# Optimization experiments

Measured on AMD Instinct MI355X. Metric: run time of the kernel, lower is better.

The kernel has to match this reference:

```python
import jax, jax.numpy as jnp
import numpy as np

# Dims: B=4 batch, S=1024 seq, E=512 embed_dim, H=8 heads, K=3 gate lookback.
_B, _S, _E, _H, _K = 4, 1024, 512, 8, 3
_EPS_LN = 1e-5
_DIV_DELTA = 1e-12


def setup_inputs() -> dict:
    key = jax.random.key(0)
    ks = jax.random.split(key, 8)

    def w(k, shape, s=0.02):
        return jax.random.normal(k, shape, jnp.float32) * s

    return {
        "query": jax.random.normal(ks[0], (_B, _S, _E), jnp.float32),
        "ln1_g": jnp.ones((_E,), jnp.float32),
        "ln1_b": jnp.zeros((_E,), jnp.float32),
        "in_proj_w": w(ks[1], (3 * _E, _E)),          # packed W_q;W_k;W_v
        "in_proj_b": jnp.zeros((3 * _E,), jnp.float32),
        "out_w": w(ks[2], (_E, _H * _E)),             # out_proj: Linear(E*H -> E)
        "out_b": jnp.zeros((_E,), jnp.float32),
        "conv_w": w(ks[3], (_H, _E, _K)),             # SyntacticDistanceGate causal conv
        "conv_b": jnp.zeros((_H,), jnp.float32),
        "ln2_g": jnp.ones((_E,), jnp.float32),
        "ln2_b": jnp.zeros((_E,), jnp.float32),
        "mlp_w1": w(ks[4], (4 * _E, _E)),
        "mlp_b1": jnp.zeros((4 * _E,), jnp.float32),
        "mlp_w2": w(ks[5], (_E, 4 * _E)),
        "mlp_b2": jnp.zeros((_E,), jnp.float32),
    }


def _layer_norm(x, g, b):
    m = jnp.mean(x, axis=-1, keepdims=True)
    v = jnp.mean(jnp.square(x - m), axis=-1, keepdims=True)
    return (x - m) * jax.lax.rsqrt(v + _EPS_LN) * g + b


def _syntactic_gate(x, conv_w, conv_b):
    """x: [B,S,E] -> gate [B,H,S,S], distance [B,H,S].
    Causal depth-to-head conv produces per-head syntactic distances; gate is a
    smooth comparison sigmoid(d_i - d_j) (PRPN-style distance gating)."""
    K = conv_w.shape[-1]
    xp = jnp.pad(x, ((0, 0), (K - 1, 0), (0, 0)))  # causal left pad
    S = x.shape[1]
    d = conv_b[None, :, None]
    for k in range(K):  # tiny fixed lookback loop
        d = d + jnp.einsum("bse,he->bhs", xp[:, k:k + S, :], conv_w[:, :, k])
    distance = jnp.tanh(d)                               # [B,H,S]
    gate = jax.nn.sigmoid(distance[:, :, :, None] - distance[:, :, None, :])
    return gate, distance


def reference(query, ln1_g, ln1_b, in_proj_w, in_proj_b, out_w, out_b,
              conv_w, conv_b, ln2_g, ln2_b, mlp_w1, mlp_b1, mlp_w2, mlp_b2):
    B, S, E = query.shape
    H = conv_w.shape[0]

    nq = _layer_norm(query, ln1_g, ln1_b)  # self-attention: key=value=normed query

    gate, _distance = _syntactic_gate(nq, conv_w, conv_b)  # [B,H,S,S]

    # In-projections (heads are NOT split: each head sees full E-dim q/k/v).
    qkv = nq @ in_proj_w.T + in_proj_b          # [B,S,3E]
    q, k, v = jnp.split(qkv, 3, axis=-1)

    # Raw scores (scaled by sqrt(E), per source). Identical across heads since
    # q/k are merely repeated per head; compute once and broadcast over H.
    scores = jnp.einsum("bie,bje->bij", q, k) / jnp.sqrt(jnp.float32(E))

    # NOTE: with no key_padding_mask the source skips softmax entirely; the
    # gate multiplies RAW scores, then sum-normalizes.
    w = scores[:, None, :, :] * gate                       # [B,H,S,S]
    w = w / (jnp.sum(w, axis=-1, keepdims=True) + _DIV_DELTA)

    ctx = jnp.einsum("bhij,bje->bhie", w, v)               # [B,H,S,E]
    # torch: chunk over head-major dim 0 then cat on features -> [B,S,H*E]
    ctx = jnp.transpose(ctx, (0, 2, 1, 3)).reshape(B, S, H * E)
    attn_out = ctx @ out_w.T + out_b                       # [B,S,E]

    x = query + attn_out                                   # layer_scale_1 = Identity
    h = _layer_norm(x, ln2_g, ln2_b)
    h = jax.nn.gelu(h @ mlp_w1.T + mlp_b1, approximate=False)
    x = x + (h @ mlp_w2.T + mlp_b2)                        # layer_scale_2 = Identity
    return x
```

## Files before the change

### kernel.cpp

```cpp
#include <hip/hip_runtime.h>
#include <math.h>

#define SQ 1024
#define EE 512
#define NB 4
#define NH 8

typedef __attribute__((ext_vector_type(8))) short bfrag;
typedef __attribute__((ext_vector_type(4))) float f32x4;
typedef __attribute__((ext_vector_type(4))) unsigned short u16x4;
typedef __attribute__((ext_vector_type(8))) unsigned short u16x8;

typedef __attribute__((address_space(3))) unsigned int lds_u32;
typedef const __attribute__((address_space(1))) unsigned int glb_u32;

__device__ __forceinline__ float sep(float x) {
  asm volatile("" : "+v"(x));
  return x;
}

__device__ __forceinline__ unsigned short f2bf(float f) {
  unsigned u = __builtin_bit_cast(unsigned, f);
  unsigned r = (u + 0x7fffu + ((u >> 16) & 1u)) >> 16;
  return (unsigned short)r;
}
__device__ __forceinline__ float bf2f(unsigned short h) {
  unsigned u = ((unsigned)h) << 16;
  return __builtin_bit_cast(float, u);
}

__device__ __forceinline__ void split4(float4 v, u16x4& h, u16x4& l) {
  h.x = f2bf(v.x); l.x = f2bf(v.x - bf2f(h.x));
  h.y = f2bf(v.y); l.y = f2bf(v.y - bf2f(h.y));
  h.z = f2bf(v.z); l.z = f2bf(v.z - bf2f(h.z));
  h.w = f2bf(v.w); l.w = f2bf(v.w - bf2f(h.w));
}

__device__ __forceinline__ int swzi(int row, int c8) {
  return row * 40 + ((c8 ^ ((row >> 2) & 6)) << 2);
}

__global__ __launch_bounds__(64) void ln_np(const float* __restrict__ x,
                                            const float* __restrict__ g,
                                            const float* __restrict__ b,
                                            float* __restrict__ y) {
  __shared__ float xs[EE];
  __shared__ float bc[2];
  long long t = blockIdx.x;
  int lane = threadIdx.x;
#pragma unroll
  for (int m = 0; m < 8; m++) xs[lane + 64 * m] = x[t * EE + lane + 64 * m];
  __syncthreads();
  int l = lane >> 3, a = lane & 7;
  float r = 0.f;
  if (lane < 32) {
    r = xs[l * 128 + a];
#pragma unroll
    for (int m = 1; m < 16; m++) r = r + xs[l * 128 + 8 * m + a];
  }
  r = r + __shfl_xor(r, 1);
  r = r + __shfl_xor(r, 2);
  r = r + __shfl_xor(r, 4);
  r = r + __shfl_xor(r, 8);
  r = r + __shfl_xor(r, 16);
  if (lane == 0) bc[0] = r / 512.0f;
  __syncthreads();
  float mean = bc[0];
  r = 0.f;
  if (lane < 32) {
#pragma unroll
    for (int m = 0; m < 16; m++) {
      float d = sep(xs[l * 128 + 8 * m + a] - mean);
      float s2 = sep(d * d);
      r = (m == 0) ? s2 : (r + s2);
    }
  }
  r = r + __shfl_xor(r, 1);
  r = r + __shfl_xor(r, 2);
  r = r + __shfl_xor(r, 4);
  r = r + __shfl_xor(r, 8);
  r = r + __shfl_xor(r, 16);
  if (lane == 0) bc[1] = r / 512.0f;
  __syncthreads();
  float var = bc[1];
  float rs = 1.0f / sqrtf(var + 1e-5f);
#pragma unroll
  for (int m = 0; m < 8; m++) {
    int i = lane + 64 * m;
    float d = sep(xs[i] - mean);
    float t1 = sep(d * rs);
    float t2 = sep(t1 * g[i]);
    y[t * EE + i] = t2 + b[i];
  }
}

__global__ __launch_bounds__(64) void ln_np_s(const float* __restrict__ x,
                                              const float* __restrict__ g,
                                              const float* __restrict__ b,
                                              unsigned short* __restrict__ yh,
                                              unsigned short* __restrict__ yl) {
  __shared__ float xs[EE];
  __shared__ float bc[2];
  long long t = blockIdx.x;
  int lane = threadIdx.x;
#pragma unroll
  for (int m = 0; m < 8; m++) xs[lane + 64 * m] = x[t * EE + lane + 64 * m];
  __syncthreads();
  int l = lane >> 3, a = lane & 7;
  float r = 0.f;
  if (lane < 32) {
    r = xs[l * 128 + a];
#pragma unroll
    for (int m = 1; m < 16; m++) r = r + xs[l * 128 + 8 * m + a];
  }
  r = r + __shfl_xor(r, 1);
  r = r + __shfl_xor(r, 2);
  r = r + __shfl_xor(r, 4);
  r = r + __shfl_xor(r, 8);
  r = r + __shfl_xor(r, 16);
  if (lane == 0) bc[0] = r / 512.0f;
  __syncthreads();
  float mean = bc[0];
  r = 0.f;
  if (lane < 32) {
#pragma unroll
    for (int m = 0; m < 16; m++) {
      float d = sep(xs[l * 128 + 8 * m + a] - mean);
      float s2 = sep(d * d);
      r = (m == 0) ? s2 : (r + s2);
    }
  }
  r = r + __shfl_xor(r, 1);
  r = r + __shfl_xor(r, 2);
  r = r + __shfl_xor(r, 4);
  r = r + __shfl_xor(r, 8);
  r = r + __shfl_xor(r, 16);
  if (lane == 0) bc[1] = r / 512.0f;
  __syncthreads();
  float var = bc[1];
  float rs = 1.0f / sqrtf(var + 1e-5f);
#pragma unroll
  for (int m = 0; m < 8; m++) {
    int i = lane + 64 * m;
    float d = sep(xs[i] - mean);
    float t1 = sep(d * rs);
    float t2 = sep(t1 * g[i]);
    float o = t2 + b[i];
    unsigned short hh = f2bf(o);
    yh[t * EE + i] = hh;
    yl[t * EE + i] = f2bf(o - bf2f(hh));
  }
}

__global__ __launch_bounds__(256) void dist_np(const float* __restrict__ nq,
                                               const float* __restrict__ conv_w,
                                               const float* __restrict__ conv_b,
                                               float* __restrict__ dist) {
  int bh = blockIdx.x;
  int b = bh >> 3, h = bh & 7;
  float cb = conv_b[h];
  const float* W = conv_w + (long long)h * EE * 3;
  int s = blockIdx.y * 256 + threadIdx.x;
  float d = cb;
#pragma unroll
  for (int k = 0; k < 3; k++) {
    int t = s - 2 + k;
    if (t < 0) continue;
    const float* row = nq + ((long long)b * SQ + t) * EE;
    float acc = 0.f;
    for (int e = 0; e < EE; e++) acc = __builtin_fmaf(row[e], W[e * 3 + k], acc);
    d = sep(d + acc);
  }
  dist[(long long)bh * SQ + s] = (float)tanh((double)d);
}

__device__ __forceinline__ float gelu_exact(float x) {
  return 0.5f * x * (1.f + erff(x / 1.41421356237309504880f));
}

template <int ACT, int SPLITK>
__global__ __launch_bounds__(256) void gemm_nt(const float* __restrict__ A, int lda, long long sA,
                                               const float* __restrict__ B, int ldb, long long sB,
                                               const float* __restrict__ bias,
                                               const float* __restrict__ Res,
                                               float* __restrict__ C, int ldc, long long sC,
                                               int K, float alpha) {
  __shared__ float As[16][68];
  __shared__ float Bs[16][68];
  int z = blockIdx.z;
  A += (long long)z * sA;
  B += (long long)z * sB;
  C += (long long)z * sC;
  int m0 = blockIdx.y * 64, n0 = blockIdx.x * 64;
  int tid = threadIdx.x;
  int lr = tid >> 2, lc = tid & 3;
  int tx = tid & 15, ty = tid >> 4;
  float acc[4][4] = {};
  float acc2[4][4] = {};
  const float* Arow = A + (long long)(m0 + lr) * lda + lc * 4;
  const float* Brow = B + (long long)(n0 + lr) * ldb + lc * 4;
  float4 a4 = *(const float4*)(Arow);
  float4 b4 = *(const float4*)(Brow);
  for (int k0 = 0; k0 < K; k0 += 16) {
    __syncthreads();
    As[lc * 4 + 0][lr] = a4.x; As[lc * 4 + 1][lr] = a4.y;
    As[lc * 4 + 2][lr] = a4.z; As[lc * 4 + 3][lr] = a4.w;
    Bs[lc * 4 + 0][lr] = b4.x; Bs[lc * 4 + 1][lr] = b4.y;
    Bs[lc * 4 + 2][lr] = b4.z; Bs[lc * 4 + 3][lr] = b4.w;
    __syncthreads();
    int kn = (k0 + 16 < K) ? (k0 + 16) : k0;
    float4 a4n = *(const float4*)(Arow + kn);
    float4 b4n = *(const float4*)(Brow + kn);
    float(*tgt)[4] = (SPLITK > 0 && k0 >= SPLITK) ? acc2 : acc;
#pragma unroll
    for (int kk = 0; kk < 16; kk++) {
      float4 av = *(const float4*)&As[kk][ty * 4];
      float4 bv = *(const float4*)&Bs[kk][tx * 4];
      float a[4] = {av.x, av.y, av.z, av.w};
      float bb[4] = {bv.x, bv.y, bv.z, bv.w};
#pragma unroll
      for (int i = 0; i < 4; i++)
#pragma unroll
        for (int j = 0; j < 4; j++) tgt[i][j] += a[i] * bb[j];
    }
    a4 = a4n;
    b4 = b4n;
  }
  if (SPLITK > 0) {
#pragma unroll
    for (int i = 0; i < 4; i++)
#pragma unroll
      for (int j = 0; j < 4; j++) acc[i][j] = sep(acc[i][j]) + acc2[i][j];
  }
  float4 bias4 = make_float4(0.f, 0.f, 0.f, 0.f);
  if (ACT != 2 && bias) bias4 = *(const float4*)(bias + n0 + tx * 4);
#pragma unroll
  for (int i = 0; i < 4; i++) {
    int row = m0 + ty * 4 + i;
    float o[4];
    if (ACT == 2) {
#pragma unroll
      for (int j = 0; j < 4; j++) o[j] = acc[i][j] / alpha;
    } else {
      o[0] = sep(acc[i][0] * alpha) + bias4.x;
      o[1] = sep(acc[i][1] * alpha) + bias4.y;
      o[2] = sep(acc[i][2] * alpha) + bias4.z;
      o[3] = sep(acc[i][3] * alpha) + bias4.w;
    }
    if (ACT == 1) {
#pragma unroll
      for (int j = 0; j < 4; j++) o[j] = gelu_exact(o[j]);
    }
    if (Res) {
      float4 r4 = *(const float4*)(Res + (long long)row * ldc + n0 + tx * 4);
      o[0] = sep(o[0]) + r4.x; o[1] = sep(o[1]) + r4.y;
      o[2] = sep(o[2]) + r4.z; o[3] = sep(o[3]) + r4.w;
    }
    *(float4*)(C + (long long)row * ldc + n0 + tx * 4) = make_float4(o[0], o[1], o[2], o[3]);
  }
}

__global__ __launch_bounds__(64) void rowsum_np(const float* __restrict__ scores,
                                                const float* __restrict__ dist,
                                                float* __restrict__ invrs) {
  __shared__ float wsm[SQ];
  int i = blockIdx.x;
  int z = blockIdx.y;
  int b = z >> 3;
  const float* srow = scores + ((long long)b * SQ + i) * SQ;
  const float* dz = dist + (long long)z * SQ;
  float di = dz[i];
  int lane = threadIdx.x;
#pragma unroll
  for (int m = 0; m < 16; m++) {
    int j = lane + 64 * m;
    float e = (float)exp((double)(dz[j] - di));
    float gg = 1.f / (1.f + e);
    wsm[j] = srow[j] * gg;
  }
  __syncthreads();
  int l = lane >> 3, a = lane & 7;
  float r = wsm[l * 128 + a];
#pragma unroll
  for (int m = 1; m < 16; m++) r = r + wsm[l * 128 + 8 * m + a];
  r = r + __shfl_xor(r, 1);
  r = r + __shfl_xor(r, 2);
  r = r + __shfl_xor(r, 4);
  r = r + __shfl_xor(r, 8);
  r = r + __shfl_xor(r, 16);
  r = r + __shfl_xor(r, 32);
  if (lane == 0) invrs[(long long)z * SQ + i] = 1.f / (r + 1e-12f);
}

__global__ __launch_bounds__(256) void vsplit_t(const float* __restrict__ qkv,
                                                unsigned short* __restrict__ VhT,
                                                unsigned short* __restrict__ VlT) {
  __shared__ float tile[64][65];
  int b = blockIdx.z;
  int j0 = blockIdx.x * 64;
  int e0 = blockIdx.y * 64;
  const float* V = qkv + (long long)b * SQ * (3 * EE) + 2 * EE;
  unsigned short* Vh = VhT + (long long)b * EE * SQ;
  unsigned short* Vl = VlT + (long long)b * EE * SQ;
  int tx = threadIdx.x & 15, ty = threadIdx.x >> 4;
#pragma unroll
  for (int r = 0; r < 4; r++) {
    int j = j0 + ty + r * 16;
    float4 v = *(const float4*)(V + (long long)j * (3 * EE) + e0 + tx * 4);
    tile[ty + r * 16][tx * 4 + 0] = v.x;
    tile[ty + r * 16][tx * 4 + 1] = v.y;
    tile[ty + r * 16][tx * 4 + 2] = v.z;
    tile[ty + r * 16][tx * 4 + 3] = v.w;
  }
  __syncthreads();
#pragma unroll
  for (int r = 0; r < 4; r++) {
    int el = ty + r * 16;
    float4 f;
    f.x = tile[tx * 4 + 0][el];
    f.y = tile[tx * 4 + 1][el];
    f.z = tile[tx * 4 + 2][el];
    f.w = tile[tx * 4 + 3][el];
    u16x4 hh, ll;
    split4(f, hh, ll);
    long long o = (long long)(e0 + el) * SQ + j0 + tx * 4;
    *(u16x4*)(Vh + o) = hh;
    *(u16x4*)(Vl + o) = ll;
  }
}

__global__ __launch_bounds__(256) void wsplit(const float* __restrict__ W,
                                              unsigned short* __restrict__ Wh,
                                              unsigned short* __restrict__ Wl, int n4) {
  int i = blockIdx.x * 256 + threadIdx.x;
  if (i >= n4) return;
  float4 v = *(const float4*)(W + (long long)i * 4);
  u16x4 h, l;
  split4(v, h, l);
  *(u16x4*)(Wh + (long long)i * 4) = h;
  *(u16x4*)(Wl + (long long)i * 4) = l;
}

__global__ __launch_bounds__(256) void ctx_bf3(const float* __restrict__ scores,
                                               const float* __restrict__ dist,
                                               const float* __restrict__ invrs,
                                               const unsigned short* __restrict__ VhT,
                                               const unsigned short* __restrict__ VlT,
                                               unsigned short* __restrict__ Ch,
                                               unsigned short* __restrict__ Cl) {
  constexpr int BN = 256;
  constexpr int NF = 4;
  __shared__ __align__(16) unsigned short Ah[64 * 40], Al[64 * 40];
  __shared__ __align__(16) unsigned short Bh[BN * 40], Bl[BN * 40];
  int z = blockIdx.z, b = z >> 3, h = z & 7;
  const float* Sb = scores + (long long)b * SQ * SQ;
  const unsigned short* Vh = VhT + (long long)b * EE * SQ;
  const unsigned short* Vl = VlT + (long long)b * EE * SQ;
  unsigned short* Chb = Ch + (long long)b * SQ * (NH * EE) + h * EE;
  unsigned short* Clb = Cl + (long long)b * SQ * (NH * EE) + h * EE;
  const float* dz = dist + (long long)z * SQ;
  int m0 = blockIdx.y * 64, n0 = blockIdx.x * BN;
  int tid = threadIdx.x;
  int wave = tid >> 6, lane = tid & 63;
  int quad = lane >> 4, l16 = lane & 15;
  int colb0 = wave * 64;
  f32x4 acc[4][NF];
#pragma unroll
  for (int mf = 0; mf < 4; mf++)
#pragma unroll
    for (int nf = 0; nf < NF; nf++) acc[mf][nf] = (f32x4)(0.f);

  int aam = tid & 63, aakc = tid >> 6;
  float di = dz[m0 + aam];
  float inv = invrs[(long long)z * SQ + m0 + aam];
  const float* Srow = Sb + (long long)(m0 + aam) * SQ;
  int brow = tid;
  const unsigned short* VhRow = Vh + (long long)(n0 + brow) * SQ;
  const unsigned short* VlRow = Vl + (long long)(n0 + brow) * SQ;

  u16x4 aH[2], aL[2];
  u16x8 bH[4], bL[4];

  auto loadconv = [&](int kb) {
#pragma unroll
    for (int r = 0; r < 2; r++) {
      int kc = aakc + r * 4;
      float4 s4 = *(const float4*)(Srow + kb + kc * 4);
      float4 d4 = *(const float4*)(dz + kb + kc * 4);
      float4 a;
      a.x = (s4.x * __builtin_amdgcn_rcpf(1.f + __expf(d4.x - di))) * inv;
      a.y = (s4.y * __builtin_amdgcn_rcpf(1.f + __expf(d4.y - di))) * inv;
      a.z = (s4.z * __builtin_amdgcn_rcpf(1.f + __expf(d4.z - di))) * inv;
      a.w = (s4.w * __builtin_amdgcn_rcpf(1.f + __expf(d4.w - di))) * inv;
      split4(a, aH[r], aL[r]);
    }
#pragma unroll
    for (int c = 0; c < 4; c++) {
      bH[c] = *(const u16x8*)(VhRow + kb + c * 8);
      bL[c] = *(const u16x8*)(VlRow + kb + c * 8);
    }
  };

  loadconv(0);
  for (int k0 = 0; k0 < SQ; k0 += 32) {
    __syncthreads();
#pragma unroll
    for (int r = 0; r < 2; r++) {
      *(u16x4*)&Ah[swzi(aam, aakc + r * 4)] = aH[r];
      *(u16x4*)&Al[swzi(aam, aakc + r * 4)] = aL[r];
    }
#pragma unroll
    for (int c = 0; c < 4; c++) {
      *(u16x8*)&Bh[swzi(brow, 2 * c)] = bH[c];
      *(u16x8*)&Bl[swzi(brow, 2 * c)] = bL[c];
    }
    __syncthreads();
    int kn = (k0 + 32 < SQ) ? (k0 + 32) : k0;
    loadconv(kn);
    bfrag bhf[NF], blf[NF];
#pragma unroll
    for (int nf = 0; nf < NF; nf++) {
      bhf[nf] = *(const bfrag*)&Bh[swzi(colb0 + nf * 16 + l16, quad * 2)];
      blf[nf] = *(const bfrag*)&Bl[swzi(colb0 + nf * 16 + l16, quad * 2)];
    }
#pragma unroll
    for (int mf = 0; mf < 4; mf++) {
      bfrag ah = *(const bfrag*)&Ah[swzi(mf * 16 + l16, quad * 2)];
      bfrag al = *(const bfrag*)&Al[swzi(mf * 16 + l16, quad * 2)];
#pragma unroll
      for (int nf = 0; nf < NF; nf++) {
        acc[mf][nf] = __builtin_amdgcn_mfma_f32_16x16x32_bf16(al, bhf[nf], acc[mf][nf], 0, 0, 0);
        acc[mf][nf] = __builtin_amdgcn_mfma_f32_16x16x32_bf16(ah, blf[nf], acc[mf][nf], 0, 0, 0);
        acc[mf][nf] = __builtin_amdgcn_mfma_f32_16x16x32_bf16(ah, bhf[nf], acc[mf][nf], 0, 0, 0);
      }
    }
  }
#pragma unroll
  for (int mf = 0; mf < 4; mf++) {
#pragma unroll
    for (int nf = 0; nf < NF; nf++) {
      int col = n0 + colb0 + nf * 16 + l16;
#pragma unroll
      for (int r = 0; r < 4; r++) {
        int row = m0 + mf * 16 + quad * 4 + r;
        float o = acc[mf][nf][r];
        unsigned short hh = f2bf(o);
        Chb[(long long)row * (NH * EE) + col] = hh;
        Clb[(long long)row * (NH * EE) + col] = f2bf(o - bf2f(hh));
      }
    }
  }
}

template <int ACT, int OUTM>
__global__ __launch_bounds__(256) void gemm_bf3s(
    const unsigned short* __restrict__ Ah_g, const unsigned short* __restrict__ Al_g, int lda,
    const unsigned short* __restrict__ Bh_g, const unsigned short* __restrict__ Bl_g, int ldb,
    const float* __restrict__ bias, const float* __restrict__ Res,
    float* __restrict__ C, unsigned short* __restrict__ Ch, unsigned short* __restrict__ Cl,
    int ldc, int K) {
  __shared__ __align__(16) unsigned short lds[3][4][64 * 32];
  int gx = gridDim.x;
  int nwg = gx * (int)gridDim.y;
  int lin = blockIdx.y * gx + blockIdx.x;
  int cpx = nwg >> 3;
  int tl = (lin & 7) * cpx + (lin >> 3);
  int bx = tl % gx, by = tl / gx;
  int m0 = by * 64, n0 = bx * 64;
  int tid = threadIdx.x, wave = tid >> 6, lane = tid & 63;
  int quad = lane >> 4, l16 = lane & 15;
  int colb0 = wave * 16;

  const unsigned short* gsrc = (wave == 0) ? Ah_g : (wave == 1) ? Al_g : (wave == 2) ? Bh_g : Bl_g;
  int gld = (wave < 2) ? lda : ldb;
  int grow0 = (wave < 2) ? m0 : n0;
  long long gbase[4];
#pragma unroll
  for (int qt = 0; qt < 4; qt++) {
    int row = qt * 16 + (lane >> 2);
    int cG = (lane & 3) ^ ((row >> 1) & 3);
    gbase[qt] = (long long)(grow0 + row) * gld + cG * 8;
  }

  auto stage = [&](int buf, int kb) {
#pragma unroll
    for (int qt = 0; qt < 4; qt++) {
      const unsigned short* gp = gsrc + gbase[qt] + kb;
      unsigned short* lp = &lds[buf][wave][qt * 512];
      __builtin_amdgcn_global_load_lds((glb_u32*)gp, (lds_u32*)lp, 16, 0, 0);
    }
  };

  int aoff[4], boff;
#pragma unroll
  for (int mf = 0; mf < 4; mf++) {
    int r = mf * 16 + l16;
    aoff[mf] = r * 32 + ((quad ^ ((r >> 1) & 3)) * 8);
  }
  {
    int r = colb0 + l16;
    boff = r * 32 + ((quad ^ ((r >> 1) & 3)) * 8);
  }

  f32x4 acc[4];
#pragma unroll
  for (int mf = 0; mf < 4; mf++) acc[mf] = (f32x4)(0.f);

  int NT = K >> 5;
  stage(0, 0);
  stage(1, 32);
  int cur = 0;
  for (int t = 0; t < NT; t++) {
    int nb = cur + 2; if (nb >= 3) nb -= 3;
    int kf = (t + 2 < NT) ? (t + 2) * 32 : (NT - 1) * 32;
    stage(nb, kf);
    asm volatile("s_waitcnt vmcnt(8)" ::: "memory");
    __builtin_amdgcn_s_barrier();
    __builtin_amdgcn_sched_barrier(0);
    const unsigned short* Lah = lds[cur][0];
    const unsigned short* Lal = lds[cur][1];
    const unsigned short* Lbh = lds[cur][2];
    const unsigned short* Lbl = lds[cur][3];
    bfrag bh = *(const bfrag*)&Lbh[boff];
    bfrag bl = *(const bfrag*)&Lbl[boff];
#pragma unroll
    for (int mf = 0; mf < 4; mf++) {
      bfrag ah = *(const bfrag*)&Lah[aoff[mf]];
      bfrag al = *(const bfrag*)&Lal[aoff[mf]];
      acc[mf] = __builtin_amdgcn_mfma_f32_16x16x32_bf16(al, bh, acc[mf], 0, 0, 0);
      acc[mf] = __builtin_amdgcn_mfma_f32_16x16x32_bf16(ah, bl, acc[mf], 0, 0, 0);
      acc[mf] = __builtin_amdgcn_mfma_f32_16x16x32_bf16(ah, bh, acc[mf], 0, 0, 0);
    }
    __builtin_amdgcn_sched_barrier(0);
    __builtin_amdgcn_s_barrier();
    cur++; if (cur >= 3) cur -= 3;
  }

  int col = n0 + colb0 + l16;
  float bi = bias ? bias[col] : 0.f;
#pragma unroll
  for (int mf = 0; mf < 4; mf++) {
#pragma unroll
    for (int r = 0; r < 4; r++) {
      int row = m0 + mf * 16 + quad * 4 + r;
      float o = acc[mf][r] + bi;
      if (ACT == 1) o = gelu_exact(o);
      if (OUTM == 0) {
        if (Res) o = o + Res[(long long)row * ldc + col];
        C[(long long)row * ldc + col] = o;
      } else {
        unsigned short hh = f2bf(o);
        Ch[(long long)row * ldc + col] = hh;
        Cl[(long long)row * ldc + col] = f2bf(o - bf2f(hh));
      }
    }
  }
}

extern "C" void kernel_launch(void* const* d_in, const int* in_sizes, int n_in,
                              void* d_out, int out_size, void* d_ws, size_t ws_size,
                              hipStream_t stream) {
  const float* query     = (const float*)d_in[0];
  const float* ln1_g     = (const float*)d_in[1];
  const float* ln1_b     = (const float*)d_in[2];
  const float* in_proj_w = (const float*)d_in[3];
  const float* in_proj_b = (const float*)d_in[4];
  const float* out_w     = (const float*)d_in[5];
  const float* out_b     = (const float*)d_in[6];
  const float* conv_w    = (const float*)d_in[7];
  const float* conv_b    = (const float*)d_in[8];
  const float* ln2_g     = (const float*)d_in[9];
  const float* ln2_b     = (const float*)d_in[10];
  const float* mlp_w1    = (const float*)d_in[11];
  const float* mlp_b1    = (const float*)d_in[12];
  const float* mlp_w2    = (const float*)d_in[13];
  const float* mlp_b2    = (const float*)d_in[14];
  float* out = (float*)d_out;
  char* ws = (char*)d_ws;

  float* nq     = (float*)(ws + 0);
  float* qkv    = (float*)(ws + (8ull << 20));
  float* dist   = (float*)(ws + (32ull << 20));
  float* invrs  = (float*)(ws + (32ull << 20) + 131072);
  float* scores = (float*)(ws + (32ull << 20) + 262144);
  unsigned short* VhT = (unsigned short*)(ws + 0);
  unsigned short* VlT = (unsigned short*)(ws + (4ull << 20));
  unsigned short* ctxh = (unsigned short*)(ws + (48ull << 20) + 262144);
  unsigned short* ctxl = (unsigned short*)(ws + (80ull << 20) + 262144);
  unsigned short* out_wh = (unsigned short*)(ws + (32ull << 20) + 262144);
  unsigned short* out_wl = out_wh + 2097152;
  unsigned short* w1h    = out_wl + 2097152;
  unsigned short* w1l    = w1h + 1048576;
  unsigned short* w2h    = w1l + 1048576;
  unsigned short* w2l    = w2h + 1048576;
  unsigned short* ln2h = (unsigned short*)(ws + (48ull << 20) + 262144);
  unsigned short* ln2l = ln2h + 2097152;
  unsigned short* hbufh = (unsigned short*)(ws + 0);
  unsigned short* hbufl = hbufh + 8388608;

  ln_np<<<dim3(NB * SQ), 64, 0, stream>>>(query, ln1_g, ln1_b, nq);
  dist_np<<<dim3(NB * NH, 4), 256, 0, stream>>>(nq, conv_w, conv_b, dist);
  gemm_nt<0, 384><<<dim3(24, 64, 1), 256, 0, stream>>>(nq, EE, 0, in_proj_w, EE, 0,
                                                       in_proj_b, nullptr, qkv, 3 * EE, 0, EE, 1.f);
  vsplit_t<<<dim3(16, 8, NB), 256, 0, stream>>>(qkv, VhT, VlT);
  gemm_nt<2, 384><<<dim3(16, 16, NB), 256, 0, stream>>>(
      qkv, 3 * EE, (long long)SQ * 3 * EE, qkv + EE, 3 * EE, (long long)SQ * 3 * EE,
      nullptr, nullptr, scores, SQ, (long long)SQ * SQ, EE, sqrtf(512.0f));
  rowsum_np<<<dim3(SQ, NB * NH), 64, 0, stream>>>(scores, dist, invrs);
  ctx_bf3<<<dim3(EE / 256, 16, NB * NH), 256, 0, stream>>>(scores, dist, invrs, VhT, VlT,
                                                           ctxh, ctxl);
  wsplit<<<dim3(2048), 256, 0, stream>>>(out_w, out_wh, out_wl, 524288);
  wsplit<<<dim3(1024), 256, 0, stream>>>(mlp_w1, w1h, w1l, 262144);
  wsplit<<<dim3(1024), 256, 0, stream>>>(mlp_w2, w2h, w2l, 262144);
  gemm_bf3s<0, 0><<<dim3(8, 64), 256, 0, stream>>>(ctxh, ctxl, NH * EE, out_wh, out_wl, NH * EE,
                                                   out_b, query, out, nullptr, nullptr,
                                                   EE, NH * EE);
  ln_np_s<<<dim3(NB * SQ), 64, 0, stream>>>(out, ln2_g, ln2_b, ln2h, ln2l);
  gemm_bf3s<1, 1><<<dim3(32, 64), 256, 0, stream>>>(ln2h, ln2l, EE, w1h, w1l, EE,
                                                    mlp_b1, nullptr, nullptr, hbufh, hbufl,
                                                    4 * EE, EE);
  gemm_bf3s<0, 0><<<dim3(8, 64), 256, 0, stream>>>(hbufh, hbufl, 4 * EE, w2h, w2l, 4 * EE,
                                                   mlp_b2, out, out, nullptr, nullptr,
                                                   EE, 4 * EE);
}
```

Measured before the change: 748.7 us.

## Enlarge ctx and bf16x3 GEMM tiles to 2x2 wave layouts for reuse

After: 730.1 us. -2.5%, faster.

```diff
diff --git a/kernel.cpp b/kernel.cpp
--- a/kernel.cpp
+++ b/kernel.cpp
@@ -348,10 +348,8 @@
                                                const unsigned short* __restrict__ VlT,
                                                unsigned short* __restrict__ Ch,
                                                unsigned short* __restrict__ Cl) {
-  constexpr int BN = 256;
-  constexpr int NF = 4;
-  __shared__ __align__(16) unsigned short Ah[64 * 40], Al[64 * 40];
-  __shared__ __align__(16) unsigned short Bh[BN * 40], Bl[BN * 40];
+  __shared__ __align__(16) unsigned short Ah[128 * 40], Al[128 * 40];
+  __shared__ __align__(16) unsigned short Bh[128 * 40], Bl[128 * 40];
   int z = blockIdx.z, b = z >> 3, h = z & 7;
   const float* Sb = scores + (long long)b * SQ * SQ;
   const unsigned short* Vh = VhT + (long long)b * EE * SQ;
@@ -359,32 +357,31 @@
   unsigned short* Chb = Ch + (long long)b * SQ * (NH * EE) + h * EE;
   unsigned short* Clb = Cl + (long long)b * SQ * (NH * EE) + h * EE;
   const float* dz = dist + (long long)z * SQ;
-  int m0 = blockIdx.y * 64, n0 = blockIdx.x * BN;
+  int m0 = blockIdx.y * 128, n0 = blockIdx.x * 128;
   int tid = threadIdx.x;
   int wave = tid >> 6, lane = tid & 63;
   int quad = lane >> 4, l16 = lane & 15;
-  int colb0 = wave * 64;
-  f32x4 acc[4][NF];
+  f32x4 acc[4][4];
 #pragma unroll
   for (int mf = 0; mf < 4; mf++)
 #pragma unroll
-    for (int nf = 0; nf < NF; nf++) acc[mf][nf] = (f32x4)(0.f);
-
-  int aam = tid & 63, aakc = tid >> 6;
+    for (int nf = 0; nf < 4; nf++) acc[mf][nf] = (f32x4)(0.f);
+
+  int aam = tid & 127, aakc = tid >> 7;
   float di = dz[m0 + aam];
   float inv = invrs[(long long)z * SQ + m0 + aam];
   const float* Srow = Sb + (long long)(m0 + aam) * SQ;
-  int brow = tid;
+  int brow = tid & 127, bk8 = tid >> 7;
   const unsigned short* VhRow = Vh + (long long)(n0 + brow) * SQ;
   const unsigned short* VlRow = Vl + (long long)(n0 + brow) * SQ;
 
-  u16x4 aH[2], aL[2];
-  u16x8 bH[4], bL[4];
+  u16x4 aH[4], aL[4];
+  u16x8 bH[2], bL[2];
 
   auto loadconv = [&](int kb) {
 #pragma unroll
-    for (int r = 0; r < 2; r++) {
-      int kc = aakc + r * 4;
+    for (int r = 0; r < 4; r++) {
+      int kc = aakc * 4 + r;
       float4 s4 = *(const float4*)(Srow + kb + kc * 4);
       float4 d4 = *(const float4*)(dz + kb + kc * 4);
       float4 a;
@@ -395,9 +392,9 @@
       split4(a, aH[r], aL[r]);
     }
 #pragma unroll
-    for (int c = 0; c < 4; c++) {
-      bH[c] = *(const u16x8*)(VhRow + kb + c * 8);
-      bL[c] = *(const u16x8*)(VlRow + kb + c * 8);
+    for (int r = 0; r < 2; r++) {
+      bH[r] = *(const u16x8*)(VhRow + kb + (bk8 * 2 + r) * 8);
+      bL[r] = *(const u16x8*)(VlRow + kb + (bk8 * 2 + r) * 8);
     }
   };
 
@@ -405,30 +402,32 @@
   for (int k0 = 0; k0 < SQ; k0 += 32) {
     __syncthreads();
 #pragma unroll
+    for (int r = 0; r < 4; r++) {
+      *(u16x4*)&Ah[swzi(aam, aakc * 4 + r)] = aH[r];
+      *(u16x4*)&Al[swzi(aam, aakc * 4 + r)] = aL[r];
+    }
+#pragma unroll
     for (int r = 0; r < 2; r++) {
-      *(u16x4*)&Ah[swzi(aam, aakc + r * 4)] = aH[r];
-      *(u16x4*)&Al[swzi(aam, aakc + r * 4)] = aL[r];
-    }
-#pragma unroll
-    for (int c = 0; c < 4; c++) {
-      *(u16x8*)&Bh[swzi(brow, 2 * c)] = bH[c];
-      *(u16x8*)&Bl[swzi(brow, 2 * c)] = bL[c];
+      *(u16x8*)&Bh[swzi(brow, (bk8 * 2 + r) * 2)] = bH[r];
+      *(u16x8*)&Bl[swzi(brow, (bk8 * 2 + r) * 2)] = bL[r];
     }
     __syncthreads();
     int kn = (k0 + 32 < SQ) ? (k0 + 32) : k0;
     loadconv(kn);
-    bfrag bhf[NF], blf[NF];
-#pragma unroll
-    for (int nf = 0; nf < NF; nf++) {
-      bhf[nf] = *(const bfrag*)&Bh[swzi(colb0 + nf * 16 + l16, quad * 2)];
-      blf[nf] = *(const bfrag*)&Bl[swzi(colb0 + nf * 16 + l16, quad * 2)];
+    bfrag bhf[4], blf[4];
+#pragma unroll
+    for (int nf = 0; nf < 4; nf++) {
+      int rb = (wave & 1) * 64 + nf * 16 + l16;
+      bhf[nf] = *(const bfrag*)&Bh[swzi(rb, quad * 2)];
+      blf[nf] = *(const bfrag*)&Bl[swzi(rb, quad * 2)];
     }
 #pragma unroll
     for (int mf = 0; mf < 4; mf++) {
-      bfrag ah = *(const bfrag*)&Ah[swzi(mf * 16 + l16, quad * 2)];
-      bfrag al = *(const bfrag*)&Al[swzi(mf * 16 + l16, quad * 2)];
-#pragma unroll
-      for (int nf = 0; nf < NF; nf++) {
+      int ra = (wave >> 1) * 64 + mf * 16 + l16;
+      bfrag ah = *(const bfrag*)&Ah[swzi(ra, quad * 2)];
+      bfrag al = *(const bfrag*)&Al[swzi(ra, quad * 2)];
+#pragma unroll
+      for (int nf = 0; nf < 4; nf++) {
         acc[mf][nf] = __builtin_amdgcn_mfma_f32_16x16x32_bf16(al, bhf[nf], acc[mf][nf], 0, 0, 0);
         acc[mf][nf] = __builtin_amdgcn_mfma_f32_16x16x32_bf16(ah, blf[nf], acc[mf][nf], 0, 0, 0);
         acc[mf][nf] = __builtin_amdgcn_mfma_f32_16x16x32_bf16(ah, bhf[nf], acc[mf][nf], 0, 0, 0);
@@ -438,11 +437,11 @@
 #pragma unroll
   for (int mf = 0; mf < 4; mf++) {
 #pragma unroll
-    for (int nf = 0; nf < NF; nf++) {
-      int col = n0 + colb0 + nf * 16 + l16;
+    for (int nf = 0; nf < 4; nf++) {
+      int col = n0 + (wave & 1) * 64 + nf * 16 + l16;
 #pragma unroll
       for (int r = 0; r < 4; r++) {
-        int row = m0 + mf * 16 + quad * 4 + r;
+        int row = m0 + (wave >> 1) * 64 + mf * 16 + quad * 4 + r;
         float o = acc[mf][nf][r];
         unsigned short hh = f2bf(o);
         Chb[(long long)row * (NH * EE) + col] = hh;
@@ -453,58 +452,64 @@
 }
 
 template <int ACT, int OUTM>
-__global__ __launch_bounds__(256) void gemm_bf3s(
+__global__ __launch_bounds__(256) void gemm_bf3w(
     const unsigned short* __restrict__ Ah_g, const unsigned short* __restrict__ Al_g, int lda,
     const unsigned short* __restrict__ Bh_g, const unsigned short* __restrict__ Bl_g, int ldb,
     const float* __restrict__ bias, const float* __restrict__ Res,
     float* __restrict__ C, unsigned short* __restrict__ Ch, unsigned short* __restrict__ Cl,
     int ldc, int K) {
-  __shared__ __align__(16) unsigned short lds[3][4][64 * 32];
+  __shared__ __align__(16) unsigned short lds[3 * 12288];
   int gx = gridDim.x;
   int nwg = gx * (int)gridDim.y;
   int lin = blockIdx.y * gx + blockIdx.x;
   int cpx = nwg >> 3;
   int tl = (lin & 7) * cpx + (lin >> 3);
   int bx = tl % gx, by = tl / gx;
-  int m0 = by * 64, n0 = bx * 64;
+  int m0 = by * 128, n0 = bx * 64;
   int tid = threadIdx.x, wave = tid >> 6, lane = tid & 63;
   int quad = lane >> 4, l16 = lane & 15;
-  int colb0 = wave * 16;
-
-  const unsigned short* gsrc = (wave == 0) ? Ah_g : (wave == 1) ? Al_g : (wave == 2) ? Bh_g : Bl_g;
-  int gld = (wave < 2) ? lda : ldb;
-  int grow0 = (wave < 2) ? m0 : n0;
-  long long gbase[4];
-#pragma unroll
-  for (int qt = 0; qt < 4; qt++) {
+
+  const unsigned short* gptr[6];
+  int ldsoff[6];
+#pragma unroll
+  for (int i = 0; i < 6; i++) {
+    int d = wave * 6 + i;
+    const unsigned short* src;
+    int rowbase, ld, tb, qt;
+    if (d < 8)       { src = Ah_g; rowbase = m0; ld = lda; tb = 0;     qt = d; }
+    else if (d < 16) { src = Al_g; rowbase = m0; ld = lda; tb = 4096;  qt = d - 8; }
+    else if (d < 20) { src = Bh_g; rowbase = n0; ld = ldb; tb = 8192;  qt = d - 16; }
+    else             { src = Bl_g; rowbase = n0; ld = ldb; tb = 10240; qt = d - 20; }
     int row = qt * 16 + (lane >> 2);
     int cG = (lane & 3) ^ ((row >> 1) & 3);
-    gbase[qt] = (long long)(grow0 + row) * gld + cG * 8;
+    gptr[i] = src + (long long)(rowbase + row) * ld + cG * 8;
+    ldsoff[i] = tb + qt * 512;
   }
 
   auto stage = [&](int buf, int kb) {
 #pragma unroll
-    for (int qt = 0; qt < 4; qt++) {
-      const unsigned short* gp = gsrc + gbase[qt] + kb;
-      unsigned short* lp = &lds[buf][wave][qt * 512];
-      __builtin_amdgcn_global_load_lds((glb_u32*)gp, (lds_u32*)lp, 16, 0, 0);
-    }
+    for (int i = 0; i < 6; i++)
+      __builtin_amdgcn_global_load_lds((glb_u32*)(gptr[i] + kb),
+                                       (lds_u32*)&lds[buf * 12288 + ldsoff[i]], 16, 0, 0);
   };
 
-  int aoff[4], boff;
+  int aoff[4], boff[2];
 #pragma unroll
   for (int mf = 0; mf < 4; mf++) {
-    int r = mf * 16 + l16;
+    int r = (wave >> 1) * 64 + mf * 16 + l16;
     aoff[mf] = r * 32 + ((quad ^ ((r >> 1) & 3)) * 8);
   }
-  {
-    int r = colb0 + l16;
-    boff = r * 32 + ((quad ^ ((r >> 1) & 3)) * 8);
-  }
-
-  f32x4 acc[4];
-#pragma unroll
-  for (int mf = 0; mf < 4; mf++) acc[mf] = (f32x4)(0.f);
+#pragma unroll
+  for (int nf = 0; nf < 2; nf++) {
+    int r = (wave & 1) * 32 + nf * 16 + l16;
+    boff[nf] = r * 32 + ((quad ^ ((r >> 1) & 3)) * 8);
+  }
+
+  f32x4 acc[4][2];
+#pragma unroll
+  for (int mf = 0; mf < 4; mf++)
+#pragma unroll
+    for (int nf = 0; nf < 2; nf++) acc[mf][nf] = (f32x4)(0.f);
 
   int NT = K >> 5;
   stage(0, 0);
@@ -514,44 +519,51 @@
     int nb = cur + 2; if (nb >= 3) nb -= 3;
     int kf = (t + 2 < NT) ? (t + 2) * 32 : (NT - 1) * 32;
     stage(nb, kf);
-    asm volatile("s_waitcnt vmcnt(8)" ::: "memory");
+    asm volatile("s_waitcnt vmcnt(12)" ::: "memory");
     __builtin_amdgcn_s_barrier();
     __builtin_amdgcn_sched_barrier(0);
-    const unsigned short* Lah = lds[cur][0];
-    const unsigned short* Lal = lds[cur][1];
-    const unsigned short* Lbh = lds[cur][2];
-    const unsigned short* Lbl = lds[cur][3];
-    bfrag bh = *(const bfrag*)&Lbh[boff];
-    bfrag bl = *(const bfrag*)&Lbl[boff];
+    const unsigned short* L = &lds[cur * 12288];
+    bfrag bh[2], bl[2];
+#pragma unroll
+    for (int nf = 0; nf < 2; nf++) {
+      bh[nf] = *(const bfrag*)&L[8192 + boff[nf]];
+      bl[nf] = *(const bfrag*)&L[10240 + boff[nf]];
+    }
 #pragma unroll
     for (int mf = 0; mf < 4; mf++) {
-      bfrag ah = *(const bfrag*)&Lah[aoff[mf]];
-      bfrag al = *(const bfrag*)&Lal[aoff[mf]];
-      acc[mf] = __builtin_amdgcn_mfma_f32_16x16x32_bf16(al, bh, acc[mf], 0, 0, 0);
-      acc[mf] = __builtin_amdgcn_mfma_f32_16x16x32_bf16(ah, bl, acc[mf], 0, 0, 0);
-      acc[mf] = __builtin_amdgcn_mfma_f32_16x16x32_bf16(ah, bh, acc[mf], 0, 0, 0);
+      bfrag ah = *(const bfrag*)&L[aoff[mf]];
+      bfrag al = *(const bfrag*)&L[4096 + aoff[mf]];
+#pragma unroll
+      for (int nf = 0; nf < 2; nf++) {
+        acc[mf][nf] = __builtin_amdgcn_mfma_f32_16x16x32_bf16(al, bh[nf], acc[mf][nf], 0, 0, 0);
+        acc[mf][nf] = __builtin_amdgcn_mfma_f32_16x16x32_bf16(ah, bl[nf], acc[mf][nf], 0, 0, 0);
+        acc[mf][nf] = __builtin_amdgcn_mfma_f32_16x16x32_bf16(ah, bh[nf], acc[mf][nf], 0, 0, 0);
+      }
     }
     __builtin_amdgcn_sched_barrier(0);
     __builtin_amdgcn_s_barrier();
     cur++; if (cur >= 3) cur -= 3;
   }
 
-  int col = n0 + colb0 + l16;
-  float bi = bias ? bias[col] : 0.f;
 #pragma unroll
   for (int mf = 0; mf < 4; mf++) {
 #pragma unroll
-    for (int r = 0; r < 4; r++) {
-      int row = m0 + mf * 16 + quad * 4 + r;
-      float o = acc[mf][r] + bi;
-      if (ACT == 1) o = gelu_exact(o);
-      if (OUTM == 0) {
-        if (Res) o = o + Res[(long long)row * ldc + col];
-        C[(long long)row * ldc + col] = o;
-      } else {
-        unsigned short hh = f2bf(o);
-        Ch[(long long)row * ldc + col] = hh;
-        Cl[(long long)row * ldc + col] = f2bf(o - bf2f(hh));
+    for (int nf = 0; nf < 2; nf++) {
+      int col = n0 + (wave & 1) * 32 + nf * 16 + l16;
+      float bi = bias ? bias[col] : 0.f;
+#pragma unroll
+      for (int r = 0; r < 4; r++) {
+        int row = m0 + (wave >> 1) * 64 + mf * 16 + quad * 4 + r;
+        float o = acc[mf][nf][r] + bi;
+        if (ACT == 1) o = gelu_exact(o);
+        if (OUTM == 0) {
+          if (Res) o = o + Res[(long long)row * ldc + col];
+          C[(long long)row * ldc + col] = o;
+        } else {
+          unsigned short hh = f2bf(o);
+          Ch[(long long)row * ldc + col] = hh;
+          Cl[(long long)row * ldc + col] = f2bf(o - bf2f(hh));
+        }
       }
     }
   }
@@ -607,19 +619,19 @@
       qkv, 3 * EE, (long long)SQ * 3 * EE, qkv + EE, 3 * EE, (long long)SQ * 3 * EE,
       nullptr, nullptr, scores, SQ, (long long)SQ * SQ, EE, sqrtf(512.0f));
   rowsum_np<<<dim3(SQ, NB * NH), 64, 0, stream>>>(scores, dist, invrs);
-  ctx_bf3<<<dim3(EE / 256, 16, NB * NH), 256, 0, stream>>>(scores, dist, invrs, VhT, VlT,
-                                                           ctxh, ctxl);
+  ctx_bf3<<<dim3(4, 8, NB * NH), 256, 0, stream>>>(scores, dist, invrs, VhT, VlT,
+                                                   ctxh, ctxl);
   wsplit<<<dim3(2048), 256, 0, stream>>>(out_w, out_wh, out_wl, 524288);
   wsplit<<<dim3(1024), 256, 0, stream>>>(mlp_w1, w1h, w1l, 262144);
   wsplit<<<dim3(1024), 256, 0, stream>>>(mlp_w2, w2h, w2l, 262144);
-  gemm_bf3s<0, 0><<<dim3(8, 64), 256, 0, stream>>>(ctxh, ctxl, NH * EE, out_wh, out_wl, NH * EE,
+  gemm_bf3w<0, 0><<<dim3(8, 32), 256, 0, stream>>>(ctxh, ctxl, NH * EE, out_wh, out_wl, NH * EE,
                                                    out_b, query, out, nullptr, nullptr,
                                                    EE, NH * EE);
   ln_np_s<<<dim3(NB * SQ), 64, 0, stream>>>(out, ln2_g, ln2_b, ln2h, ln2l);
-  gemm_bf3s<1, 1><<<dim3(32, 64), 256, 0, stream>>>(ln2h, ln2l, EE, w1h, w1l, EE,
+  gemm_bf3w<1, 1><<<dim3(32, 32), 256, 0, stream>>>(ln2h, ln2l, EE, w1h, w1l, EE,
                                                     mlp_b1, nullptr, nullptr, hbufh, hbufl,
                                                     4 * EE, EE);
-  gemm_bf3s<0, 0><<<dim3(8, 64), 256, 0, stream>>>(hbufh, hbufl, 4 * EE, w2h, w2l, 4 * EE,
+  gemm_bf3w<0, 0><<<dim3(8, 32), 256, 0, stream>>>(hbufh, hbufl, 4 * EE, w2h, w2l, 4 * EE,
                                                    mlp_b2, out, out, nullptr, nullptr,
                                                    EE, 4 * EE);
 }
```
